# Kernel optimization log

Hardware: AMD Instinct MI355X
Metric: run time of the kernel (lower is better)

## Reference

```python
import jax, jax.numpy as jnp
import numpy as np

B, S, D = 32, 1024, 1025  # batch, seq_length(=num_loci), input_dim
QD, KD = 64, 64
INIT_SCALE = 0.03


def _attention(y, Wq, Wk, Wv):
    # y: [B, S, D]
    q = jnp.einsum('bsd,dq->bsq', y, Wq)
    k = jnp.einsum('bsd,dk->bsk', y, Wk)
    v = jnp.einsum('bsd,de->bse', y, Wv)
    scores = jax.nn.softmax(jnp.einsum('bsq,btq->bst', q, k), axis=-1)
    return jnp.einsum('bst,bte->bse', scores, v)


def setup_inputs() -> dict:
    key = jax.random.key(0)
    ks = jax.random.split(key, 13)
    p = lambda k, shape: INIT_SCALE * jax.random.normal(k, shape, dtype=jnp.float32)
    return {
        'x': jax.random.normal(ks[0], (B, S, D), dtype=jnp.float32),
        'Wq1': p(ks[1], (D, QD)), 'Wk1': p(ks[2], (D, KD)), 'Wv1': p(ks[3], (D, D)),
        'Wq2': p(ks[4], (D, QD)), 'Wk2': p(ks[5], (D, KD)), 'Wv2': p(ks[6], (D, D)),
        'Wq3': p(ks[7], (D, QD)), 'Wk3': p(ks[8], (D, KD)), 'Wv3': p(ks[9], (D, D)),
        'random_matrix': p(ks[10], (S, D - 1)),
        'coeffs_attended': p(ks[11], (S, D)),
        'offset': p(ks[12], (1,)),
    }


def reference(x, Wq1, Wk1, Wv1, Wq2, Wk2, Wv2, Wq3, Wk3, Wv3,
              random_matrix, coeffs_attended, offset):
    # y = concat(x[:, :, :S] @ random_matrix, x[:, :, -1:])  -> [B, S, D]
    y = jnp.concatenate(
        [jnp.einsum('bsf,fe->bse', x[:, :, :S], random_matrix), x[:, :, -1:]],
        axis=2)
    a1 = _attention(y, Wq1, Wk1, Wv1)
    a2 = _attention(a1, Wq2, Wk2, Wv2)
    a3 = _attention(a2, Wq3, Wk3, Wv3)
    out = jnp.einsum('bij,ij->b', a3, coeffs_attended) + offset
    return out
```

## Files before the change

### kernel.cpp

```cpp
#include <hip/hip_runtime.h>
#include <hip/hip_bf16.h>
#include <stdint.h>

typedef __bf16 bf16;
typedef __bf16 bf16x8 __attribute__((ext_vector_type(8)));
typedef float f32x4 __attribute__((ext_vector_type(4)));
typedef float f32x8u __attribute__((ext_vector_type(8)));
typedef f32x8u f32x8a __attribute__((aligned(4)));

__device__ __forceinline__ void gl16(const void* g, void* lds) {
  __builtin_amdgcn_global_load_lds(
      (const __attribute__((address_space(1))) void*)g,
      (__attribute__((address_space(3))) void*)lds, 16, 0, 0);
}

template <int OUT>
__global__ __launch_bounds__(256) void gemm_hr(
    const bf16* __restrict__ Ah, const bf16* __restrict__ Ar, int lda,
    long long sA_, const bf16* __restrict__ Bh, const bf16* __restrict__ Br,
    int ldb, long long sB_, float* __restrict__ Cf, bf16* __restrict__ Ch,
    bf16* __restrict__ Cr, int ldc, long long sC_, int N, int K, int ntn) {
  __shared__ bf16 tAh[128][32], tAr[128][32], tBh[128][32], tBr[128][32];

  const int tid = threadIdx.x;
  const int lane = tid & 63, wave = tid >> 6;
  const int wm = wave & 1, wn = wave >> 1;
  const int fr = lane & 15, fq = lane >> 4;

  const long long bz = blockIdx.y;
  Ah += bz * sA_;
  Ar += bz * sA_;
  Bh += bz * sB_;
  Br += bz * sB_;

  const int cpx = gridDim.x >> 3;
  const int b2 = (blockIdx.x & 7) * cpx + (blockIdx.x >> 3);
  const int tm = b2 / ntn, tn = b2 % ntn;
  const int m0 = tm * 128, n0 = tn * 128;

  const int c0 = wave * 128 + lane;
  const int colsw = (((c0 & 3) ^ ((c0 >> 3) & 3)) << 3);
  const int rA0 = m0 + (c0 >> 2);
  int rB0 = n0 + (c0 >> 2), rB1 = rB0 + 16;
  rB0 = rB0 < N ? rB0 : N - 1;
  rB1 = rB1 < N ? rB1 : N - 1;
  const long long offA0 = (long long)rA0 * lda + colsw;
  const long long offA1 = offA0 + (long long)16 * lda;
  const long long offB0 = (long long)rB0 * ldb + colsw;
  const long long offB1 = (long long)rB1 * ldb + colsw;

  char* dAh = (char*)&tAh[0][0] + wave * 2048;
  char* dAr = (char*)&tAr[0][0] + wave * 2048;
  char* dBh = (char*)&tBh[0][0] + wave * 2048;
  char* dBr = (char*)&tBr[0][0] + wave * 2048;

  const int colA = ((fq ^ ((fr >> 1) & 3)) << 3);

  f32x4 acc[4][4] = {};
  const int nk = K >> 5;
  for (int kt = 0; kt < nk; ++kt) {
    const int k0 = kt << 5;
    gl16(Ah + offA0 + k0, dAh);
    gl16(Ah + offA1 + k0, dAh + 1024);
    gl16(Ar + offA0 + k0, dAr);
    gl16(Ar + offA1 + k0, dAr + 1024);
    gl16(Bh + offB0 + k0, dBh);
    gl16(Bh + offB1 + k0, dBh + 1024);
    gl16(Br + offB0 + k0, dBr);
    gl16(Br + offB1 + k0, dBr + 1024);
    __syncthreads();

    bf16x8 ah[4], ar_[4], bh[4], br_[4];
#pragma unroll
    for (int i = 0; i < 4; ++i) {
      ah[i] = *reinterpret_cast<const bf16x8*>(&tAh[wm * 64 + i * 16 + fr][colA]);
      ar_[i] = *reinterpret_cast<const bf16x8*>(&tAr[wm * 64 + i * 16 + fr][colA]);
      bh[i] = *reinterpret_cast<const bf16x8*>(&tBh[wn * 64 + i * 16 + fr][colA]);
      br_[i] = *reinterpret_cast<const bf16x8*>(&tBr[wn * 64 + i * 16 + fr][colA]);
    }
#pragma unroll
    for (int mi = 0; mi < 4; ++mi)
#pragma unroll
      for (int ni = 0; ni < 4; ++ni)
        acc[mi][ni] = __builtin_amdgcn_mfma_f32_16x16x32_bf16(
            ah[mi], bh[ni], acc[mi][ni], 0, 0, 0);
#pragma unroll
    for (int mi = 0; mi < 4; ++mi)
#pragma unroll
      for (int ni = 0; ni < 4; ++ni)
        acc[mi][ni] = __builtin_amdgcn_mfma_f32_16x16x32_bf16(
            ah[mi], br_[ni], acc[mi][ni], 0, 0, 0);
#pragma unroll
    for (int mi = 0; mi < 4; ++mi)
#pragma unroll
      for (int ni = 0; ni < 4; ++ni)
        acc[mi][ni] = __builtin_amdgcn_mfma_f32_16x16x32_bf16(
            ar_[mi], bh[ni], acc[mi][ni], 0, 0, 0);
    __syncthreads();
  }

  if constexpr (OUT == 0) {
    float* C = Cf + bz * sC_;
#pragma unroll
    for (int mi = 0; mi < 4; ++mi)
#pragma unroll
      for (int ni = 0; ni < 4; ++ni) {
        int cc = n0 + wn * 64 + ni * 16 + fr;
        if (cc < N) {
          long long base = (long long)(m0 + wm * 64 + mi * 16 + fq * 4) * ldc + cc;
#pragma unroll
          for (int j = 0; j < 4; ++j) C[base + (long long)j * ldc] = acc[mi][ni][j];
        }
      }
  } else {
    bf16* CH = Ch + bz * sC_;
    bf16* CR = Cr + bz * sC_;
#pragma unroll
    for (int mi = 0; mi < 4; ++mi)
#pragma unroll
      for (int ni = 0; ni < 4; ++ni) {
        int cc = n0 + wn * 64 + ni * 16 + fr;
        if (cc < N) {
          long long base = (long long)(m0 + wm * 64 + mi * 16 + fq * 4) * ldc + cc;
#pragma unroll
          for (int j = 0; j < 4; ++j) {
            float v = acc[mi][ni][j];
            bf16 h = (bf16)v;
            CH[base + (long long)j * ldc] = h;
            CR[base + (long long)j * ldc] = (bf16)(v - (float)h);
          }
        }
      }
  }
}

template <int OUT>
__global__ __launch_bounds__(256, 2) void gemm_hr2(
    const bf16* __restrict__ Ah, const bf16* __restrict__ Ar, int lda,
    long long sA_, const bf16* __restrict__ Bh, const bf16* __restrict__ Br,
    int ldb, long long sB_, float* __restrict__ Cf, bf16* __restrict__ Ch,
    bf16* __restrict__ Cr, int ldc, long long sC_, int N, int K, int ntn) {
  __shared__ bf16 tAh[256][32], tAr[256][32], tBh[128][32], tBr[128][32];

  const int tid = threadIdx.x;
  const int lane = tid & 63, wave = tid >> 6;
  const int wm = wave & 1, wn = wave >> 1;
  const int fr = lane & 15, fq = lane >> 4;

  const long long bz = blockIdx.y;
  Ah += bz * sA_;
  Ar += bz * sA_;
  Bh += bz * sB_;
  Br += bz * sB_;

  const int nwg = gridDim.x;
  const int q = nwg >> 3, r = nwg & 7;
  const int xcd = blockIdx.x & 7, o8 = blockIdx.x >> 3;
  const int b2 = (xcd < r ? xcd * (q + 1) : r * (q + 1) + (xcd - r) * q) + o8;
  const int tm = b2 / ntn, tn = b2 % ntn;
  const int m0 = tm * 256, n0 = tn * 128;

  const int cA = wave * 64 + lane;
  const int colsw = (((cA & 3) ^ ((cA >> 3) & 3)) << 3);
  const int rA = cA >> 2;
  const long long offA = (long long)(m0 + rA) * lda + colsw;
  const long long strA = (long long)64 * lda;
  int rB0 = n0 + rA, rB1 = n0 + rA + 64;
  rB0 = rB0 < N ? rB0 : N - 1;
  rB1 = rB1 < N ? rB1 : N - 1;
  const long long offB0 = (long long)rB0 * ldb + colsw;
  const long long offB1 = (long long)rB1 * ldb + colsw;

  char* dAh = (char*)&tAh[0][0] + wave * 1024;
  char* dAr = (char*)&tAr[0][0] + wave * 1024;
  char* dBh = (char*)&tBh[0][0] + wave * 1024;
  char* dBr = (char*)&tBr[0][0] + wave * 1024;

  const int colA = ((fq ^ ((fr >> 1) & 3)) << 3);

  f32x4 acc[8][4] = {};
  const int nk = K >> 5;
  for (int kt = 0; kt < nk; ++kt) {
    const int k0 = kt << 5;
#pragma unroll
    for (int j = 0; j < 4; ++j) {
      gl16(Ah + offA + j * strA + k0, dAh + j * 4096);
      gl16(Ar + offA + j * strA + k0, dAr + j * 4096);
    }
    gl16(Bh + offB0 + k0, dBh);
    gl16(Bh + offB1 + k0, dBh + 4096);
    gl16(Br + offB0 + k0, dBr);
    gl16(Br + offB1 + k0, dBr + 4096);
    __syncthreads();

    bf16x8 bh[4], br_[4];
#pragma unroll
    for (int i = 0; i < 4; ++i) {
      bh[i] = *reinterpret_cast<const bf16x8*>(&tBh[wn * 64 + i * 16 + fr][colA]);
      br_[i] = *reinterpret_cast<const bf16x8*>(&tBr[wn * 64 + i * 16 + fr][colA]);
    }
#pragma unroll
    for (int mi = 0; mi < 8; ++mi) {
      bf16x8 ah = *reinterpret_cast<const bf16x8*>(
          &tAh[wm * 128 + mi * 16 + fr][colA]);
      bf16x8 ar_ = *reinterpret_cast<const bf16x8*>(
          &tAr[wm * 128 + mi * 16 + fr][colA]);
#pragma unroll
      for (int ni = 0; ni < 4; ++ni)
        acc[mi][ni] = __builtin_amdgcn_mfma_f32_16x16x32_bf16(
            ah, bh[ni], acc[mi][ni], 0, 0, 0);
#pragma unroll
      for (int ni = 0; ni < 4; ++ni)
        acc[mi][ni] = __builtin_amdgcn_mfma_f32_16x16x32_bf16(
            ah, br_[ni], acc[mi][ni], 0, 0, 0);
#pragma unroll
      for (int ni = 0; ni < 4; ++ni)
        acc[mi][ni] = __builtin_amdgcn_mfma_f32_16x16x32_bf16(
            ar_, bh[ni], acc[mi][ni], 0, 0, 0);
    }
    __syncthreads();
  }

  if constexpr (OUT == 0) {
    float* C = Cf + bz * sC_;
#pragma unroll
    for (int mi = 0; mi < 8; ++mi)
#pragma unroll
      for (int ni = 0; ni < 4; ++ni) {
        int cc = n0 + wn * 64 + ni * 16 + fr;
        if (cc < N) {
          long long base =
              (long long)(m0 + wm * 128 + mi * 16 + fq * 4) * ldc + cc;
#pragma unroll
          for (int j = 0; j < 4; ++j) C[base + (long long)j * ldc] = acc[mi][ni][j];
        }
      }
  } else if constexpr (OUT == 1) {
    bf16* CH = Ch + bz * sC_;
    bf16* CR = Cr + bz * sC_;
#pragma unroll
    for (int mi = 0; mi < 8; ++mi)
#pragma unroll
      for (int ni = 0; ni < 4; ++ni) {
        int cc = n0 + wn * 64 + ni * 16 + fr;
        if (cc < N) {
          long long base =
              (long long)(m0 + wm * 128 + mi * 16 + fq * 4) * ldc + cc;
#pragma unroll
          for (int j = 0; j < 4; ++j) {
            float v = acc[mi][ni][j];
            bf16 h = (bf16)v;
            CH[base + (long long)j * ldc] = h;
            CR[base + (long long)j * ldc] = (bf16)(v - (float)h);
          }
        }
      }
  } else {
    bf16* CH = Ch + bz * sC_;
    bf16* CR = Cr + bz * sC_;
#pragma unroll
    for (int mi = 0; mi < 8; ++mi)
#pragma unroll
      for (int ni = 0; ni < 4; ++ni) {
        int cc = n0 + wn * 64 + ni * 16 + fr;
        if (cc < N) {
          int mr = m0 + wm * 128 + mi * 16 + fq * 4;
          union { bf16 h[4]; uint2 u; } th, tr;
#pragma unroll
          for (int j = 0; j < 4; ++j) {
            float v = acc[mi][ni][j];
            bf16 h = (bf16)v;
            th.h[j] = h;
            tr.h[j] = (bf16)(v - (float)h);
          }
          *reinterpret_cast<uint2*>(CH + (long long)cc * ldc + mr) = th.u;
          *reinterpret_cast<uint2*>(CR + (long long)cc * ldc + mr) = tr.u;
        }
      }
  }
}

__global__ __launch_bounds__(256, 2) void gemm_dot1(
    const bf16* __restrict__ Ah, int lda, long long sA_,
    const bf16* __restrict__ Bh, int ldb, long long sB_, int N, int K,
    int ntn, const float* __restrict__ G, int ldg,
    float* __restrict__ partial) {
  __shared__ bf16 tAh[256][32], tBh[128][32];

  const int tid = threadIdx.x;
  const int lane = tid & 63, wave = tid >> 6;
  const int wm = wave & 1, wn = wave >> 1;
  const int fr = lane & 15, fq = lane >> 4;

  const long long bz = blockIdx.y;
  Ah += bz * sA_;
  Bh += bz * sB_;

  const int nwg = gridDim.x;
  const int q = nwg >> 3, r = nwg & 7;
  const int xcd = blockIdx.x & 7, o8 = blockIdx.x >> 3;
  const int b2 = (xcd < r ? xcd * (q + 1) : r * (q + 1) + (xcd - r) * q) + o8;
  const int tm = b2 / ntn, tn = b2 % ntn;
  const int m0 = tm * 256, n0 = tn * 128;

  const int cA = wave * 64 + lane;
  const int colsw = (((cA & 3) ^ ((cA >> 3) & 3)) << 3);
  const int rA = cA >> 2;
  const long long offA = (long long)(m0 + rA) * lda + colsw;
  const long long strA = (long long)64 * lda;
  int rB0 = n0 + rA, rB1 = n0 + rA + 64;
  rB0 = rB0 < N ? rB0 : N - 1;
  rB1 = rB1 < N ? rB1 : N - 1;
  const long long offB0 = (long long)rB0 * ldb + colsw;
  const long long offB1 = (long long)rB1 * ldb + colsw;

  char* dAh = (char*)&tAh[0][0] + wave * 1024;
  char* dBh = (char*)&tBh[0][0] + wave * 1024;

  const int colA = ((fq ^ ((fr >> 1) & 3)) << 3);

  f32x4 acc[8][4] = {};
  const int nk = K >> 5;
  for (int kt = 0; kt < nk; ++kt) {
    const int k0 = kt << 5;
#pragma unroll
    for (int j = 0; j < 4; ++j) gl16(Ah + offA + j * strA + k0, dAh + j * 4096);
    gl16(Bh + offB0 + k0, dBh);
    gl16(Bh + offB1 + k0, dBh + 4096);
    __syncthreads();

    bf16x8 bh[4];
#pragma unroll
    for (int i = 0; i < 4; ++i)
      bh[i] = *reinterpret_cast<const bf16x8*>(&tBh[wn * 64 + i * 16 + fr][colA]);
#pragma unroll
    for (int mi = 0; mi < 8; ++mi) {
      bf16x8 ah = *reinterpret_cast<const bf16x8*>(
          &tAh[wm * 128 + mi * 16 + fr][colA]);
#pragma unroll
      for (int ni = 0; ni < 4; ++ni)
        acc[mi][ni] = __builtin_amdgcn_mfma_f32_16x16x32_bf16(
            ah, bh[ni], acc[mi][ni], 0, 0, 0);
    }
    __syncthreads();
  }

  float dot = 0.f;
#pragma unroll
  for (int mi = 0; mi < 8; ++mi)
#pragma unroll
    for (int ni = 0; ni < 4; ++ni) {
      int cc = n0 + wn * 64 + ni * 16 + fr;
      if (cc < N) {
        long long base =
            (long long)(m0 + wm * 128 + mi * 16 + fq * 4) * ldg + cc;
#pragma unroll
        for (int j = 0; j < 4; ++j)
          dot += acc[mi][ni][j] * G[base + (long long)j * ldg];
      }
    }
#pragma unroll
  for (int o = 32; o; o >>= 1) dot += __shfl_xor(dot, o);
  float* red = (float*)&tAh[0][0];
  if (lane == 0) red[wave] = dot;
  __syncthreads();
  if (tid == 0)
    partial[bz * gridDim.x + b2] = red[0] + red[1] + red[2] + red[3];
}

__global__ __launch_bounds__(256, 2) void gemm0w(
    const float* __restrict__ A, int lda, const float* __restrict__ B, int ldb,
    bf16* __restrict__ Ch, bf16* __restrict__ Cr, int ldc, int N, int K,
    int ntn) {
  __shared__ bf16 tAh[256][32], tAr[256][32], tBh[128][32], tBr[128][32];

  const int tid = threadIdx.x;
  const int lane = tid & 63, wave = tid >> 6;
  const int wm = wave & 1, wn = wave >> 1;
  const int fr = lane & 15, fq = lane >> 4;

  const int nwg = gridDim.x;
  const int q = nwg >> 3, r = nwg & 7;
  const int xcd = blockIdx.x & 7, o8 = blockIdx.x >> 3;
  const int b2 = (xcd < r ? xcd * (q + 1) : r * (q + 1) + (xcd - r) * q) + o8;
  const int tm = b2 / ntn, tn = b2 % ntn;
  const int m0 = tm * 256, n0 = tn * 128;

  const int row0 = tid >> 2, slot = tid & 3;
  const int wcol = ((slot ^ ((tid >> 3) & 3)) << 3);
  const int colA = ((fq ^ ((fr >> 1) & 3)) << 3);

  f32x4 acc[8][4] = {};
  const int nk = K >> 5;
  for (int kt = 0; kt < nk; ++kt) {
    const int k0 = kt << 5;
    f32x8a ra[4], rb[2];
#pragma unroll
    for (int p = 0; p < 4; ++p) {
      int row = row0 + p * 64;
      ra[p] = *reinterpret_cast<const f32x8a*>(
          A + (long long)(m0 + row) * lda + k0 + slot * 8);
    }
#pragma unroll
    for (int p = 0; p < 2; ++p) {
      int n = n0 + row0 + p * 64;
      n = n < N ? n : N - 1;
      rb[p] = *reinterpret_cast<const f32x8a*>(
          B + (long long)n * ldb + k0 + slot * 8);
    }
    __syncthreads();
#pragma unroll
    for (int p = 0; p < 4; ++p) {
      int row = row0 + p * 64;
      bf16x8 vh, vr;
#pragma unroll
      for (int j = 0; j < 8; ++j) {
        float f = ra[p][j];
        bf16 h = (bf16)f;
        vh[j] = h;
        vr[j] = (bf16)(f - (float)h);
      }
      *reinterpret_cast<bf16x8*>(&tAh[row][wcol]) = vh;
      *reinterpret_cast<bf16x8*>(&tAr[row][wcol]) = vr;
    }
#pragma unroll
    for (int p = 0; p < 2; ++p) {
      int row = row0 + p * 64;
      bf16x8 vh, vr;
#pragma unroll
      for (int j = 0; j < 8; ++j) {
        float f = rb[p][j];
        bf16 h = (bf16)f;
        vh[j] = h;
        vr[j] = (bf16)(f - (float)h);
      }
      *reinterpret_cast<bf16x8*>(&tBh[row][wcol]) = vh;
      *reinterpret_cast<bf16x8*>(&tBr[row][wcol]) = vr;
    }
    __syncthreads();

    bf16x8 bh[4], br_[4];
#pragma unroll
    for (int i = 0; i < 4; ++i) {
      bh[i] = *reinterpret_cast<const bf16x8*>(&tBh[wn * 64 + i * 16 + fr][colA]);
      br_[i] = *reinterpret_cast<const bf16x8*>(&tBr[wn * 64 + i * 16 + fr][colA]);
    }
#pragma unroll
    for (int mi = 0; mi < 8; ++mi) {
      bf16x8 ah = *reinterpret_cast<const bf16x8*>(
          &tAh[wm * 128 + mi * 16 + fr][colA]);
      bf16x8 ar_ = *reinterpret_cast<const bf16x8*>(
          &tAr[wm * 128 + mi * 16 + fr][colA]);
#pragma unroll
      for (int ni = 0; ni < 4; ++ni)
        acc[mi][ni] = __builtin_amdgcn_mfma_f32_16x16x32_bf16(
            ah, bh[ni], acc[mi][ni], 0, 0, 0);
#pragma unroll
      for (int ni = 0; ni < 4; ++ni)
        acc[mi][ni] = __builtin_amdgcn_mfma_f32_16x16x32_bf16(
            ah, br_[ni], acc[mi][ni], 0, 0, 0);
#pragma unroll
      for (int ni = 0; ni < 4; ++ni)
        acc[mi][ni] = __builtin_amdgcn_mfma_f32_16x16x32_bf16(
            ar_, bh[ni], acc[mi][ni], 0, 0, 0);
    }
  }

#pragma unroll
  for (int mi = 0; mi < 8; ++mi)
#pragma unroll
    for (int ni = 0; ni < 4; ++ni) {
      int cc = n0 + wn * 64 + ni * 16 + fr;
      if (cc < N) {
        long long base =
            (long long)(m0 + wm * 128 + mi * 16 + fq * 4) * ldc + cc;
#pragma unroll
        for (int j = 0; j < 4; ++j) {
          float v = acc[mi][ni][j];
          bf16 h = (bf16)v;
          Ch[base + (long long)j * ldc] = h;
          Cr[base + (long long)j * ldc] = (bf16)(v - (float)h);
        }
      }
    }
}

template <int SPLIT>
__global__ __launch_bounds__(256) void transpose_tile(
    const float* __restrict__ src, int R, int Cc, float* __restrict__ df,
    bf16* __restrict__ dh, bf16* __restrict__ dr, int Nout, int outC,
    int ntk) {
  __shared__ float t[32][33];
  const int nt = blockIdx.x / ntk, kt = blockIdx.x % ntk;
  const int n0 = nt * 32, k0 = kt * 32;
  const int c = threadIdx.x & 31, r0 = threadIdx.x >> 5;
#pragma unroll
  for (int p = 0; p < 4; ++p) {
    int k = k0 + r0 + p * 8, n = n0 + c;
    t[r0 + p * 8][c] = (k < R && n < Cc) ? src[(long long)k * Cc + n] : 0.f;
  }
  __syncthreads();
#pragma unroll
  for (int p = 0; p < 4; ++p) {
    int n = n0 + r0 + p * 8, k = k0 + c;
    if (n < Nout && k < outC) {
      float v = t[c][r0 + p * 8];
      long long idx = (long long)n * outC + k;
      if constexpr (SPLIT) {
        bf16 h = (bf16)v;
        dh[idx] = h;
        dr[idx] = (bf16)(v - (float)h);
      } else {
        df[idx] = v;
      }
    }
  }
}

__global__ __launch_bounds__(256) void transpose_h(
    const ushort* __restrict__ sh, ushort* __restrict__ dh) {
  __shared__ ushort lh[32][33];
  const long long b = blockIdx.y;
  const int et = blockIdx.x >> 5, tt = blockIdx.x & 31;
  const int e0 = et * 32, t0 = tt * 32;
  const int c = threadIdx.x & 31, r0 = threadIdx.x >> 5;
  const ushort* sh_b = sh + b * 1024 * 1056;
#pragma unroll
  for (int p = 0; p < 4; ++p) {
    int t = t0 + r0 + p * 8;
    lh[r0 + p * 8][c] = sh_b[(long long)t * 1056 + e0 + c];
  }
  __syncthreads();
  ushort* dh_b = dh + b * 1056 * 1024;
#pragma unroll
  for (int p = 0; p < 4; ++p) {
    int e = e0 + r0 + p * 8;
    dh_b[(long long)e * 1024 + t0 + c] = lh[c][r0 + p * 8];
  }
}

__global__ __launch_bounds__(256) void pad_split_g(
    const float* __restrict__ src, int R, int Cc, bf16* __restrict__ dh,
    bf16* __restrict__ dr, long long total, int outC) {
  long long idx = (long long)blockIdx.x * 256 + threadIdx.x;
  if (idx >= total) return;
  int n = (int)(idx / outC), k = (int)(idx % outC);
  float v = (n < R && k < Cc) ? src[(long long)n * Cc + k] : 0.f;
  bf16 h = (bf16)v;
  dh[idx] = h;
  dr[idx] = (bf16)(v - (float)h);
}

__global__ __launch_bounds__(256) void fixup_y_split(bf16* __restrict__ Yh,
                                                     bf16* __restrict__ Yr,
                                                     const float* __restrict__ x) {
  int row = blockIdx.x * 256 + threadIdx.x;
  if (row < 32768) {
    float v = x[(long long)row * 1025 + 1024];
    bf16 h = (bf16)v;
    long long base = (long long)row * 1056;
    Yh[base + 1024] = h;
    Yr[base + 1024] = (bf16)(v - (float)h);
#pragma unroll
    for (int c = 1025; c < 1056; ++c) {
      Yh[base + c] = (bf16)0.f;
      Yr[base + c] = (bf16)0.f;
    }
  }
}

__global__ __launch_bounds__(256) void softmax_split(
    const float* __restrict__ Plog, bf16* __restrict__ Ph,
    bf16* __restrict__ Pr, int wr) {
  long long row = blockIdx.x;
  const float* p = Plog + row * 1024;
  int tid = threadIdx.x;
  float v[4];
#pragma unroll
  for (int j = 0; j < 4; ++j) v[j] = p[tid + 256 * j];
  float m = fmaxf(fmaxf(v[0], v[1]), fmaxf(v[2], v[3]));
#pragma unroll
  for (int o = 32; o; o >>= 1) m = fmaxf(m, __shfl_xor(m, o));
  __shared__ float sm[4];
  if ((tid & 63) == 0) sm[tid >> 6] = m;
  __syncthreads();
  m = fmaxf(fmaxf(sm[0], sm[1]), fmaxf(sm[2], sm[3]));
  float s = 0.f;
#pragma unroll
  for (int j = 0; j < 4; ++j) {
    v[j] = __expf(v[j] - m);
    s += v[j];
  }
#pragma unroll
  for (int o = 32; o; o >>= 1) s += __shfl_xor(s, o);
  __shared__ float ss[4];
  if ((tid & 63) == 0) ss[tid >> 6] = s;
  __syncthreads();
  s = ss[0] + ss[1] + ss[2] + ss[3];
  float inv = 1.0f / s;
#pragma unroll
  for (int j = 0; j < 4; ++j) {
    float pv = v[j] * inv;
    bf16 h = (bf16)pv;
    Ph[row * 1024 + tid + 256 * j] = h;
    if (wr) Pr[row * 1024 + tid + 256 * j] = (bf16)(pv - (float)h);
  }
}

__global__ void finalize_k(const float* __restrict__ partial,
                           const float* __restrict__ offs,
                           float* __restrict__ out, int per_b) {
  int b = threadIdx.x;
  if (b < 32) {
    float s = 0.f;
    for (int i = 0; i < per_b; ++i) s += partial[b * per_b + i];
    out[b] = s + offs[0];
  }
}


extern "C" void kernel_launch(void* const* d_in, const int* in_sizes, int n_in,
                              void* d_out, int out_size, void* d_ws,
                              size_t ws_size, hipStream_t stream) {
  const float* x = (const float*)d_in[0];
  const float* Wq[3] = {(const float*)d_in[1], (const float*)d_in[4],
                        (const float*)d_in[7]};
  const float* Wk[3] = {(const float*)d_in[2], (const float*)d_in[5],
                        (const float*)d_in[8]};
  const float* Wv[3] = {(const float*)d_in[3], (const float*)d_in[6],
                        (const float*)d_in[9]};
  const float* R = (const float*)d_in[10];
  const float* coef = (const float*)d_in[11];
  const float* offs = (const float*)d_in[12];
  float* out = (float*)d_out;

  const int CB = (ws_size >= (size_t)390000000ULL) ? 16 : 8;
  const int NCH = 32 / CB;

  char* ws = (char*)d_ws;
  size_t off = 0;
  auto alloc = [&](size_t bytes) -> void* {
    void* p = ws + off;
    off = (off + bytes + 255) & ~(size_t)255;
    return p;
  };
  bf16* Yh = (bf16*)alloc(32768LL * 1056 * 2);
  bf16* Yr = (bf16*)alloc(32768LL * 1056 * 2);
  bf16* qkh = (bf16*)alloc(32768LL * 128 * 2);
  bf16* qkr = (bf16*)alloc(32768LL * 128 * 2);
  float* Plog = (float*)alloc((long long)CB * 1024 * 1024 * 4);
  bf16* Ph = (bf16*)alloc((long long)CB * 1024 * 1024 * 2);
  bf16* Pr = (bf16*)alloc((long long)CB * 1024 * 1024 * 2);
  bf16* vTh = (bf16*)alloc((long long)CB * 1056 * 1024 * 2);
  bf16* vTr = (bf16*)alloc((long long)CB * 1056 * 1024 * 2);
  float* RT = (float*)alloc(1024LL * 1024 * 4);
  bf16 *WqkTh[3], *WqkTr[3], *WvTh[3], *WvTr[3];
  for (int i = 0; i < 3; ++i) {
    WqkTh[i] = (bf16*)alloc(128LL * 1056 * 2);
    WqkTr[i] = (bf16*)alloc(128LL * 1056 * 2);
    WvTh[i] = (bf16*)alloc(1056LL * 1056 * 2);
    WvTr[i] = (bf16*)alloc(1056LL * 1056 * 2);
  }
  bf16* coefh = (bf16*)alloc(1024LL * 1056 * 2);
  bf16* coefr = (bf16*)alloc(1024LL * 1056 * 2);
  float* G = (float*)alloc(1024LL * 1056 * 4);
  float* partial = (float*)alloc(32 * 36 * 4);

  transpose_tile<0><<<32 * 32, 256, 0, stream>>>(R, 1024, 1024, RT, nullptr,
                                                 nullptr, 1024, 1024, 32);
  for (int l = 0; l < 3; ++l) {
    transpose_tile<1><<<33 * 2, 256, 0, stream>>>(
        Wq[l], 1025, 64, nullptr, WqkTh[l], WqkTr[l], 64, 1056, 33);
    transpose_tile<1><<<33 * 2, 256, 0, stream>>>(
        Wk[l], 1025, 64, nullptr, WqkTh[l] + 64 * 1056, WqkTr[l] + 64 * 1056,
        64, 1056, 33);
    if (l < 2) {
      transpose_tile<1><<<33 * 33, 256, 0, stream>>>(
          Wv[l], 1025, 1025, nullptr, WvTh[l], WvTr[l], 1056, 1056, 33);
    } else {
      pad_split_g<<<4356, 256, 0, stream>>>(Wv[l], 1025, 1025, WvTh[l],
                                            WvTr[l], 1056LL * 1056, 1056);
    }
  }
  pad_split_g<<<4224, 256, 0, stream>>>(coef, 1024, 1025, coefh, coefr,
                                        1024LL * 1056, 1056);
  gemm_hr<0><<<dim3(72, 1), 256, 0, stream>>>(
      coefh, coefr, 1056, 0, WvTh[2], WvTr[2], 1056, 0, G, nullptr, nullptr,
      1056, 0, 1056, 1056, 9);

  gemm0w<<<dim3(1024, 1), 256, 0, stream>>>(x, 1025, RT, 1024, Yh, Yr, 1056,
                                            1024, 1024, 8);
  fixup_y_split<<<128, 256, 0, stream>>>(Yh, Yr, x);

  for (int l = 0; l < 3; ++l) {
    gemm_hr<1><<<dim3(256, 1), 256, 0, stream>>>(
        Yh, Yr, 1056, 0, WqkTh[l], WqkTr[l], 1056, 0, nullptr, qkh, qkr, 128,
        0, 128, 1056, 1);
    for (int ch = 0; ch < NCH; ++ch) {
      const long long b0 = (long long)ch * CB;
      bf16* Ych = Yh + b0 * 1024 * 1056;
      bf16* Ycr = Yr + b0 * 1024 * 1056;
      bf16* qkch = qkh + b0 * 1024 * 128;
      bf16* qkcr = qkr + b0 * 1024 * 128;
      if (l < 2) {
        gemm_hr2<2><<<dim3(36, CB), 256, 0, stream>>>(
            Ych, Ycr, 1056, 1024LL * 1056, WvTh[l], WvTr[l], 1056, 0, nullptr,
            vTh, vTr, 1024, 1056LL * 1024, 1056, 1056, 9);
      } else {
        transpose_h<<<dim3(33 * 32, CB), 256, 0, stream>>>(
            (const ushort*)Ych, (ushort*)vTh);
      }
      gemm_hr2<0><<<dim3(32, CB), 256, 0, stream>>>(
          qkch, qkcr, 128, 1024LL * 128, qkch + 64, qkcr + 64, 128,
          1024LL * 128, Plog, nullptr, nullptr, 1024, 1024LL * 1024, 1024, 64,
          8);
      softmax_split<<<CB * 1024, 256, 0, stream>>>(Plog, Ph, Pr, l < 2 ? 1 : 0);
      if (l < 2) {
        gemm_hr2<1><<<dim3(36, CB), 256, 0, stream>>>(
            Ph, Pr, 1024, 1024LL * 1024, vTh, vTr, 1024, 1056LL * 1024,
            nullptr, Ych, Ycr, 1056, 1024LL * 1056, 1056, 1024, 9);
      } else {
        gemm_dot1<<<dim3(36, CB), 256, 0, stream>>>(
            Ph, 1024, 1024LL * 1024, vTh, 1024, 1056LL * 1024, 1056, 1024, 9,
            G, 1056, partial + b0 * 36);
      }
    }
  }

  finalize_k<<<1, 32, 0, stream>>>(partial, offs, out, 36);
}
```

Measured before the change: 2.280 ms.

## Write softmax bf16 split in place over logits buffer and enlarge batch chunks

The softmax kernel now writes its bf16 high and residual outputs in place into the float logits row: each row's 4 KB holds the 1024 high values followed by the 1024 residuals. It also switches to vectorized 16-byte loads and 8-byte stores with a contiguous per-thread layout. The downstream GEMMs read P with a leading dimension of 2048. Freeing the separate Ph/Pr buffers lets the chunk size grow to 32 batches when the workspace allows, which cuts the number of launches per layer. In-place writing is safe because each block reads its whole row before the barriers, but the larger chunk depends on the workspace size.

```diff
diff --git a/kernel.cpp b/kernel.cpp
--- a/kernel.cpp
+++ b/kernel.cpp
@@ -569,15 +569,12 @@
   }
 }
 
-__global__ __launch_bounds__(256) void softmax_split(
-    const float* __restrict__ Plog, bf16* __restrict__ Ph,
-    bf16* __restrict__ Pr, int wr) {
+__global__ __launch_bounds__(256) void softmax_split(float* __restrict__ Plog,
+                                                     int wr) {
   long long row = blockIdx.x;
-  const float* p = Plog + row * 1024;
+  float* p = Plog + row * 1024;
   int tid = threadIdx.x;
-  float v[4];
-#pragma unroll
-  for (int j = 0; j < 4; ++j) v[j] = p[tid + 256 * j];
+  f32x4 v = *reinterpret_cast<const f32x4*>(p + tid * 4);
   float m = fmaxf(fmaxf(v[0], v[1]), fmaxf(v[2], v[3]));
 #pragma unroll
   for (int o = 32; o; o >>= 1) m = fmaxf(m, __shfl_xor(m, o));
@@ -586,10 +583,11 @@
   __syncthreads();
   m = fmaxf(fmaxf(sm[0], sm[1]), fmaxf(sm[2], sm[3]));
   float s = 0.f;
+  f32x4 e;
 #pragma unroll
   for (int j = 0; j < 4; ++j) {
-    v[j] = __expf(v[j] - m);
-    s += v[j];
+    e[j] = __expf(v[j] - m);
+    s += e[j];
   }
 #pragma unroll
   for (int o = 32; o; o >>= 1) s += __shfl_xor(s, o);
@@ -598,13 +596,18 @@
   __syncthreads();
   s = ss[0] + ss[1] + ss[2] + ss[3];
   float inv = 1.0f / s;
+  bf16* ph = reinterpret_cast<bf16*>(p);
+  bf16* pr = ph + 1024;
+  union { bf16 h[4]; ushort4 u; } th, tr;
 #pragma unroll
   for (int j = 0; j < 4; ++j) {
-    float pv = v[j] * inv;
+    float pv = e[j] * inv;
     bf16 h = (bf16)pv;
-    Ph[row * 1024 + tid + 256 * j] = h;
-    if (wr) Pr[row * 1024 + tid + 256 * j] = (bf16)(pv - (float)h);
-  }
+    th.h[j] = h;
+    tr.h[j] = (bf16)(pv - (float)h);
+  }
+  *reinterpret_cast<ushort4*>(ph + tid * 4) = th.u;
+  if (wr) *reinterpret_cast<ushort4*>(pr + tid * 4) = tr.u;
 }
 
 __global__ void finalize_k(const float* __restrict__ partial,
@@ -634,7 +637,9 @@
   const float* offs = (const float*)d_in[12];
   float* out = (float*)d_out;
 
-  const int CB = (ws_size >= (size_t)390000000ULL) ? 16 : 8;
+  const int CB = (ws_size >= (size_t)470000000ULL)
+                     ? 32
+                     : ((ws_size >= (size_t)335000000ULL) ? 16 : 8);
   const int NCH = 32 / CB;
 
   char* ws = (char*)d_ws;
@@ -649,8 +654,8 @@
   bf16* qkh = (bf16*)alloc(32768LL * 128 * 2);
   bf16* qkr = (bf16*)alloc(32768LL * 128 * 2);
   float* Plog = (float*)alloc((long long)CB * 1024 * 1024 * 4);
-  bf16* Ph = (bf16*)alloc((long long)CB * 1024 * 1024 * 2);
-  bf16* Pr = (bf16*)alloc((long long)CB * 1024 * 1024 * 2);
+  bf16* Ph = (bf16*)Plog;
+  bf16* Pr = Ph + 1024;
   bf16* vTh = (bf16*)alloc((long long)CB * 1056 * 1024 * 2);
   bf16* vTr = (bf16*)alloc((long long)CB * 1056 * 1024 * 2);
   float* RT = (float*)alloc(1024LL * 1024 * 4);
@@ -714,14 +719,14 @@
           qkch, qkcr, 128, 1024LL * 128, qkch + 64, qkcr + 64, 128,
           1024LL * 128, Plog, nullptr, nullptr, 1024, 1024LL * 1024, 1024, 64,
           8);
-      softmax_split<<<CB * 1024, 256, 0, stream>>>(Plog, Ph, Pr, l < 2 ? 1 : 0);
+      softmax_split<<<CB * 1024, 256, 0, stream>>>(Plog, l < 2 ? 1 : 0);
       if (l < 2) {
         gemm_hr2<1><<<dim3(36, CB), 256, 0, stream>>>(
-            Ph, Pr, 1024, 1024LL * 1024, vTh, vTr, 1024, 1056LL * 1024,
+            Ph, Pr, 2048, 1024LL * 2048, vTh, vTr, 1024, 1056LL * 1024,
             nullptr, Ych, Ycr, 1056, 1024LL * 1056, 1056, 1024, 9);
       } else {
         gemm_dot1<<<dim3(36, CB), 256, 0, stream>>>(
-            Ph, 1024, 1024LL * 1024, vTh, 1024, 1056LL * 1024, 1056, 1024, 9,
+            Ph, 2048, 1024LL * 2048, vTh, 1024, 1056LL * 1024, 1056, 1024, 9,
             G, 1056, partial + b0 * 36);
       }
     }
```

Measured after the change: 1.933 ms. 15.2% less time.
